# Performance work log

Measured on AMD Instinct MI355X. Metric: run time of the kernel, lower is better.

The kernel has to match this reference:

```python
import jax, jax.numpy as jnp
import numpy as np

B, T, E, H = 2, 2048, 1024, 16


def setup_inputs() -> dict:
    key = jax.random.key(0)
    ks = jax.random.split(key, 8)
    # VarianceScaling(1.0) ~ truncated normal with stddev ~ sqrt(1/fan_in)
    std = 1.0 / np.sqrt(E)
    x = jax.random.normal(ks[0], (B, T, E), dtype=jnp.float32)
    y = jax.random.normal(ks[1], (B, T, E), dtype=jnp.float32)
    # causal mask [1, 1, T, T]
    mask = jnp.tril(jnp.ones((T, T), dtype=jnp.float32))[None, None]
    Wq = jax.random.normal(ks[2], (E, E), dtype=jnp.float32) * std
    Wk = jax.random.normal(ks[3], (E, E), dtype=jnp.float32) * std
    Wv = jax.random.normal(ks[4], (E, E), dtype=jnp.float32) * std
    Wo = jax.random.normal(ks[5], (E, E), dtype=jnp.float32) * std
    bq = jnp.zeros((E,), jnp.float32)
    bk = jnp.zeros((E,), jnp.float32)
    bv = jnp.zeros((E,), jnp.float32)
    bo = jnp.zeros((E,), jnp.float32)
    return {"x": x, "y": y, "mask": mask, "Wq": Wq, "bq": bq,
            "Wk": Wk, "bk": bk, "Wv": Wv, "bv": bv, "Wo": Wo, "bo": bo,
            "num_heads": H}


def reference(x, y, mask, Wq, bq, Wk, bk, Wv, bv, Wo, bo, num_heads):
    Bx, Tq, Emb = x.shape
    Tkv = y.shape[1]
    d = Emb // num_heads
    q = (x @ Wq + bq).reshape(Bx, Tq, num_heads, d)
    k = (y @ Wk + bk).reshape(Bx, Tkv, num_heads, d)
    v = (y @ Wv + bv).reshape(Bx, Tkv, num_heads, d)
    scale = 1.0 / np.sqrt(d).astype(np.float32)
    att = scale * jnp.einsum('bthd,bThd->bhtT', q, k)  # [B,H,Tq,Tkv]
    att = att * mask - 1e10 * (1.0 - mask)
    att = jax.nn.softmax(att, axis=-1)
    out = jnp.einsum('bhtT,bThd->bthd', att, v).reshape(Bx, Tq, Emb)
    return out @ Wo + bo
```

## Files before the change

kernel.cpp:

```cpp
#include <hip/hip_runtime.h>
#include <stdint.h>

#define BB 2
#define TT 2048
#define EE 1024
#define HH 16
#define DD 64
#define MM (BB*TT)

typedef unsigned short u16;
typedef __attribute__((ext_vector_type(4))) float f32x4;
typedef __attribute__((ext_vector_type(8))) __bf16 bf16x8;
typedef __attribute__((ext_vector_type(8))) u16 u16x8;
typedef __attribute__((ext_vector_type(4))) u16 u16x4;

union FragU { u16x8 u; bf16x8 b; };
union BfU { __bf16 h; u16 u; };

__device__ __forceinline__ u16 f2bf(float f) {
  uint32_t u = __float_as_uint(f);
  u += 0x7fffu + ((u >> 16) & 1u);
  return (u16)(u >> 16);
}

__device__ __forceinline__ void gload16(const u16* __restrict__ g, u16* l) {
  __builtin_amdgcn_global_load_lds((const __attribute__((address_space(1))) void*)g,
                                   (__attribute__((address_space(3))) void*)l, 16, 0, 0);
}

__global__ __launch_bounds__(256) void prep(const float* __restrict__ x, const float* __restrict__ y,
                                            const float* __restrict__ Wq, const float* __restrict__ Wk,
                                            const float* __restrict__ Wv, const float* __restrict__ Wo,
                                            u16* __restrict__ xb, u16* __restrict__ yb,
                                            u16* __restrict__ Wqt, u16* __restrict__ Wkvt,
                                            u16* __restrict__ Wot) {
  __shared__ alignas(16) float tile[64][65];
  int bi = blockIdx.x, t = threadIdx.x;
  if (bi < 4096) {
    const float* src = (bi < 2048) ? x : y;
    u16* dst = (bi < 2048) ? xb : yb;
    int i = (bi & 2047) * 256 + t;
    const f32x4* s4 = (const f32x4*)src;
    f32x4 a = s4[2*i], b = s4[2*i+1];
    u16x8 o;
    o[0]=f2bf(a[0]); o[1]=f2bf(a[1]); o[2]=f2bf(a[2]); o[3]=f2bf(a[3]);
    o[4]=f2bf(b[0]); o[5]=f2bf(b[1]); o[6]=f2bf(b[2]); o[7]=f2bf(b[3]);
    ((u16x8*)dst)[i] = o;
    return;
  }
  int wi = bi - 4096;
  int z = wi >> 8;
  const float* W; u16* Tp;
  switch (z) {
    case 0: W = Wq; Tp = Wqt; break;
    case 1: W = Wk; Tp = Wkvt; break;
    case 2: W = Wv; Tp = Wkvt + (size_t)1024*EE; break;
    default: W = Wo; Tp = Wot; break;
  }
  int r8 = wi & 255;
  int n0 = (r8 & 15) * 64, k0 = (r8 >> 4) * 64;
#pragma unroll
  for (int i = 0; i < 16; ++i) {
    int idx = i*256 + t; int r = idx >> 6, c = idx & 63;
    tile[r][c] = W[(size_t)(k0 + r) * EE + n0 + c];
  }
  __syncthreads();
#pragma unroll
  for (int i = 0; i < 16; ++i) {
    int idx = i*256 + t; int rn = idx >> 6, ck = idx & 63;
    Tp[(size_t)(n0 + rn) * EE + k0 + ck] = f2bf(tile[ck][rn]);
  }
}

template <int BM, int EPI>
__device__ __forceinline__ void gemm_body(const u16* __restrict__ A, const u16* __restrict__ Bt,
                                          const float* __restrict__ bias, void* __restrict__ Cout,
                                          int N, int K, float oscale, int bm, int bn,
                                          u16 (*As)[64], u16 (*Bs)[64]) {
  constexpr int MI = (BM + 31) / 32;
  const int t = threadIdx.x;
  const int lane = t & 63, w = t >> 6;
  const int wr = w >> 1, wc = w & 1;
  const int g = lane >> 4, cl = lane & 15;

  f32x4 acc[MI][4] = {};

  const u16* Ag = A + (size_t)(bm * BM) * K;
  const u16* Bg = Bt + (size_t)(bn * 128) * K;

  const int rl = lane >> 3;
  const int sw = ((lane & 7) ^ rl) * 8;

  const int nk = K / 64;
  for (int kt = 0; kt < nk; ++kt) {
    const int k0 = kt * 64;
    __syncthreads();
    if (BM == 32) {
      gload16(Ag + (size_t)(w*8 + rl) * K + k0 + sw, &As[w*8][0]);
    } else {
#pragma unroll
      for (int j = 0; j < MI; ++j) {
        int ca = w * MI + j;
        gload16(Ag + (size_t)(ca*8 + rl) * K + k0 + sw, &As[ca*8][0]);
      }
    }
#pragma unroll
    for (int j = 0; j < 4; ++j) {
      int cb = w * 4 + j;
      gload16(Bg + (size_t)(cb*8 + rl) * K + k0 + sw, &Bs[cb*8][0]);
    }
    __syncthreads();
#pragma unroll
    for (int ks = 0; ks < 2; ++ks) {
      FragU af[MI], bfr[4];
#pragma unroll
      for (int mi = 0; mi < MI; ++mi) {
        int row = (BM == 32) ? (wr*16 + cl) : (wr*(BM/2) + mi*16 + cl);
        af[mi].u = *(const u16x8*)&As[row][((ks*4 + g) ^ (row & 7)) * 8];
      }
#pragma unroll
      for (int nj = 0; nj < 4; ++nj) {
        int row = wc*64 + nj*16 + cl;
        bfr[nj].u = *(const u16x8*)&Bs[row][((ks*4 + g) ^ (row & 7)) * 8];
      }
#pragma unroll
      for (int mi = 0; mi < MI; ++mi)
#pragma unroll
        for (int nj = 0; nj < 4; ++nj)
          acc[mi][nj] = __builtin_amdgcn_mfma_f32_16x16x32_bf16(af[mi].b, bfr[nj].b, acc[mi][nj], 0, 0, 0);
    }
  }

  const int cbase = bn*128 + wc*64 + cl;
  float bv[4];
#pragma unroll
  for (int nj = 0; nj < 4; ++nj) bv[nj] = bias[cbase + nj*16];
#pragma unroll
  for (int mi = 0; mi < MI; ++mi) {
    int row0 = (BM == 32) ? (bm*32 + wr*16 + (g << 2))
                          : (bm*BM + wr*(BM/2) + mi*16 + (g << 2));
    if (EPI == 2) {
      int bb = row0 >> 11;
      int tt = row0 & 2047;
      int tb64 = tt & ~63;
      int w6 = tt & 63;
      int p = ((w6 >> 5) << 5) | (((w6 >> 2) & 3) << 3) | (((w6 >> 4) & 1) << 2);
#pragma unroll
      for (int nj = 0; nj < 4; ++nj) {
        int cc = cbase + nj*16;
        int hh = cc >> 6, dd = cc & 63;
        u16x4 v;
#pragma unroll
        for (int i = 0; i < 4; ++i) v[i] = f2bf(acc[mi][nj][i] + bv[nj]);
        *(u16x4*)((u16*)Cout + ((size_t)((bb*HH + hh)*DD + dd))*2048 + tb64 + p) = v;
      }
    } else {
#pragma unroll
      for (int i = 0; i < 4; ++i) {
        if (EPI == 1) {
          float* Cp = (float*)Cout + (size_t)(row0 + i) * N + cbase;
#pragma unroll
          for (int nj = 0; nj < 4; ++nj)
            Cp[nj*16] = (acc[mi][nj][i] + bv[nj]) * oscale;
        } else {
          u16* Cp = (u16*)Cout + (size_t)(row0 + i) * N + cbase;
#pragma unroll
          for (int nj = 0; nj < 4; ++nj)
            Cp[nj*16] = f2bf((acc[mi][nj][i] + bv[nj]) * oscale);
        }
      }
    }
  }
}

__global__ __launch_bounds__(256) void gemm_qkv(const u16* __restrict__ xb, const u16* __restrict__ yb,
                                                const u16* __restrict__ Wqt, const u16* __restrict__ Wkvt,
                                                const float* __restrict__ bq, const float* __restrict__ bk,
                                                const float* __restrict__ bv,
                                                u16* __restrict__ Qb, u16* __restrict__ Kb,
                                                u16* __restrict__ Vtb, float c1) {
  __shared__ alignas(16) u16 As[64][64];
  __shared__ alignas(16) u16 Bs[128][64];
  const int i = blockIdx.x;
  const int l = (i & 7) * 192 + (i >> 3);
  const int bm = l / 24, bx = l % 24;
  if (bx < 8)
    gemm_body<64, 0>(xb, Wqt, bq, Qb, 1024, EE, c1, bm, bx, As, Bs);
  else if (bx < 16)
    gemm_body<64, 0>(yb, Wkvt, bk, Kb, 1024, EE, 1.0f, bm, bx - 8, As, Bs);
  else
    gemm_body<64, 2>(yb, Wkvt + (size_t)1024*EE, bv, Vtb, 1024, EE, 1.0f, bm, bx - 16, As, Bs);
}

__global__ __launch_bounds__(256) void gemm_o(const u16* __restrict__ Atb, const u16* __restrict__ Wot,
                                              const float* __restrict__ bo, float* __restrict__ out) {
  __shared__ alignas(16) u16 As[32][64];
  __shared__ alignas(16) u16 Bs[128][64];
  const int i = blockIdx.x;
  const int l = (i & 7) * 128 + (i >> 3);
  const int bm = l / 8, bn = l % 8;
  gemm_body<32, 1>(Atb, Wot, bo, out, 1024, EE, 1.0f, bm, bn, As, Bs);
}

__global__ __launch_bounds__(512, 4) void attn(const u16* __restrict__ Q, const u16* __restrict__ Kb,
                                               const u16* __restrict__ Vt, u16* __restrict__ O) {
  const int i0 = blockIdx.x;
  const int qp = i0 >> 5;
  const int bh = i0 & 31;
  const int b = bh >> 4, h = bh & 15;

  const int t = threadIdx.x, lane = t & 63, w = t >> 6;
  const int ws_ = w & 3;
  const int hi = w >> 2;
  const int g = lane >> 4, c = lane & 15;
  __shared__ alignas(16) u16 Ks[2][2][64][64];
  __shared__ alignas(16) u16 Vs[2][2][64][64];

  const u16* Kbase = Kb + (size_t)(b*TT) * 1024 + h*DD;
  const u16* Vtbase = Vt + (size_t)(b*HH + h) * DD * 2048;

  const int rl = lane >> 3;
  const int sw = ((lane & 7) ^ rl) * 8;
  const int rowb = w*8 + rl;
  const int rxor = (c & 7);

  FragU onef;
#pragma unroll
  for (int e = 0; e < 8; ++e) onef.u[e] = 0x3F80;

  for (int pi = 0; pi < 2; ++pi) {
    const int qt = pi ? 31 - qp : qp;
    const int qw0 = qt * 64 + ws_ * 16;

    FragU qf[2];
    const u16* Qbase = Q + ((size_t)(b*TT) + qw0) * EE + h*DD;
#pragma unroll
    for (int ks = 0; ks < 2; ++ks)
      qf[ks].u = *(const u16x8*)(Qbase + (size_t)c * EE + ks*32 + g*8);

    f32x4 oacc[4] = {};
    f32x4 lacc = {};

    const int nkv = qt + 1;
    const int npair = (nkv + 1) >> 1;

    __syncthreads();
    gload16(Kbase + (size_t)rowb * 1024 + sw, &Ks[0][0][w*8][0]);
    gload16(Vtbase + (size_t)rowb * 2048 + sw, &Vs[0][0][w*8][0]);
    if (1 < nkv) {
      gload16(Kbase + (size_t)(64 + rowb) * 1024 + sw, &Ks[0][1][w*8][0]);
      gload16(Vtbase + (size_t)rowb * 2048 + 64 + sw, &Vs[0][1][w*8][0]);
    }
    __syncthreads();

    for (int jj = 0; jj < npair; ++jj) {
      const int d = jj & 1;
      const int j0 = 2*jj;
      if (jj + 1 < npair) {
        const int kvn = (j0 + 2) * 64;
        gload16(Kbase + (size_t)(kvn + rowb) * 1024 + sw, &Ks[d^1][0][w*8][0]);
        gload16(Vtbase + (size_t)rowb * 2048 + kvn + sw, &Vs[d^1][0][w*8][0]);
        if (j0 + 3 < nkv) {
          gload16(Kbase + (size_t)(kvn + 64 + rowb) * 1024 + sw, &Ks[d^1][1][w*8][0]);
          gload16(Vtbase + (size_t)rowb * 2048 + kvn + 64 + sw, &Vs[d^1][1][w*8][0]);
        }
      }

      const int j = j0 + hi;
      const int kv0 = j * 64;
      if (j < nkv && kv0 <= qw0 + 15) {
        f32x4 s[4] = {};
        __builtin_amdgcn_s_setprio(1);
#pragma unroll
        for (int ks = 0; ks < 2; ++ks) {
          const int kc = ((ks*4 + g) ^ rxor) * 8;
          FragU kf[4];
#pragma unroll
          for (int nj = 0; nj < 4; ++nj)
            kf[nj].u = *(const u16x8*)&Ks[d][hi][nj*16 + c][kc];
#pragma unroll
          for (int nj = 0; nj < 4; ++nj)
            s[nj] = __builtin_amdgcn_mfma_f32_16x16x32_bf16(kf[nj].b, qf[ks].b, s[nj], 0, 0, 0);
        }
        __builtin_amdgcn_s_setprio(0);

        const bool full = (kv0 + 63 <= qw0);
        if (!full) {
          const int q = qw0 + c;
#pragma unroll
          for (int nj = 0; nj < 4; ++nj)
#pragma unroll
            for (int r = 0; r < 4; ++r)
              if (kv0 + nj*16 + 4*g + r > q) s[nj][r] = -1e30f;
        }

        FragU pa[2];
#pragma unroll
        for (int nj = 0; nj < 4; ++nj)
#pragma unroll
          for (int r = 0; r < 4; ++r) {
            float p = exp2f(s[nj][r]);
            BfU cv; cv.h = (__bf16)p;
            pa[nj >> 1].u[(nj & 1) * 4 + r] = cv.u;
          }

        __builtin_amdgcn_s_setprio(1);
#pragma unroll
        for (int ks = 0; ks < 2; ++ks) {
          const int vc = ((ks*4 + g) ^ rxor) * 8;
#pragma unroll
          for (int dj = 0; dj < 4; ++dj) {
            FragU vf;
            vf.u = *(const u16x8*)&Vs[d][hi][dj*16 + c][vc];
            oacc[dj] = __builtin_amdgcn_mfma_f32_16x16x32_bf16(pa[ks].b, vf.b, oacc[dj], 0, 0, 0);
          }
          lacc = __builtin_amdgcn_mfma_f32_16x16x32_bf16(pa[ks].b, onef.b, lacc, 0, 0, 0);
        }
        __builtin_amdgcn_s_setprio(0);
      }

      if (jj + 1 < npair)
        __syncthreads();
    }

    __syncthreads();
    float* mO = (float*)&Ks[0][0][0][0];
    float* mL = (float*)&Vs[0][0][0][0];

    if (hi) {
#pragma unroll
      for (int i = 0; i < 4; ++i) {
        int row = 4*g + i;
#pragma unroll
        for (int dj = 0; dj < 4; ++dj)
          mO[((size_t)(ws_*16 + row))*66 + dj*16 + c] = oacc[dj][i];
      }
      if (c == 0) {
#pragma unroll
        for (int i = 0; i < 4; ++i) mL[ws_*16 + 4*g + i] = lacc[i];
      }
    }
    __syncthreads();
    if (!hi) {
      u16* Ob = O + ((size_t)(b*TT) + qw0) * EE + h*DD;
#pragma unroll
      for (int i = 0; i < 4; ++i) {
        int row = 4*g + i;
        float inv = 1.f / (lacc[i] + mL[ws_*16 + row]);
#pragma unroll
        for (int dj = 0; dj < 4; ++dj) {
          float o1 = mO[((size_t)(ws_*16 + row))*66 + dj*16 + c];
          Ob[(size_t)row * EE + dj*16 + c] = f2bf((oacc[dj][i] + o1) * inv);
        }
      }
    }
  }
}

extern "C" void kernel_launch(void* const* d_in, const int* in_sizes, int n_in,
                              void* d_out, int out_size, void* d_ws, size_t ws_size,
                              hipStream_t stream) {
  const float* x  = (const float*)d_in[0];
  const float* y  = (const float*)d_in[1];
  const float* Wq = (const float*)d_in[3];
  const float* bq = (const float*)d_in[4];
  const float* Wk = (const float*)d_in[5];
  const float* bk = (const float*)d_in[6];
  const float* Wv = (const float*)d_in[7];
  const float* bv = (const float*)d_in[8];
  const float* Wo = (const float*)d_in[9];
  const float* bo = (const float*)d_in[10];

  if (ws_size < (size_t)58720256) return;

  char* ws = (char*)d_ws;
  u16* Wqt  = (u16*)(ws + 0);
  u16* Wkvt = (u16*)(ws + 2097152);
  u16* Wot  = (u16*)(ws + 6291456);
  u16* Qb   = (u16*)(ws + 8388608);
  u16* Kb   = (u16*)(ws + 16777216);
  u16* Vtb  = (u16*)(ws + 25165824);
  u16* Atb  = (u16*)(ws + 33554432);
  u16* xb   = (u16*)(ws + 41943040);
  u16* yb   = (u16*)(ws + 50331648);

  const float c1 = 0.125f * 1.44269504088896340736f;

  prep<<<5120, 256, 0, stream>>>(x, y, Wq, Wk, Wv, Wo, xb, yb, Wqt, Wkvt, Wot);
  gemm_qkv<<<1536, 256, 0, stream>>>(xb, yb, Wqt, Wkvt, bq, bk, bv, Qb, Kb, Vtb, c1);
  attn<<<512, 512, 0, stream>>>(Qb, Kb, Vtb, Atb);
  gemm_o<<<1024, 256, 0, stream>>>(Atb, Wot, bo, (float*)d_out);
}
```

Measured before the change: 101.8 us.

## Software-pipeline PV matmul one tile behind QK in attention loop

Defers the P·V MFMA of each KV tile to the next iteration, so it runs after the next tile's Q·K^T. This lets the exp/convert work and the matmuls interleave and hide latency. The V shared buffer grows to three slots so the previous tile's V stays valid while the next one is prefetched. The cost is more LDS per block, which may reduce occupancy, plus extra register pressure from carrying the P fragments across iterations.

```diff
diff --git a/kernel.cpp b/kernel.cpp
--- a/kernel.cpp
+++ b/kernel.cpp
@@ -214,7 +214,7 @@
   const int hi = w >> 2;
   const int g = lane >> 4, c = lane & 15;
   __shared__ alignas(16) u16 Ks[2][2][64][64];
-  __shared__ alignas(16) u16 Vs[2][2][64][64];
+  __shared__ alignas(16) u16 Vs[3][2][64][64];
 
   const u16* Kbase = Kb + (size_t)(b*TT) * 1024 + h*DD;
   const u16* Vtbase = Vt + (size_t)(b*HH + h) * DD * 2048;
@@ -253,23 +253,31 @@
     }
     __syncthreads();
 
+    FragU paP[2];
+    int vslotP = 0;
+    bool haveP = false;
+
+    int vs = 0;
     for (int jj = 0; jj < npair; ++jj) {
       const int d = jj & 1;
       const int j0 = 2*jj;
+      const int vsn = (vs == 2) ? 0 : vs + 1;
       if (jj + 1 < npair) {
         const int kvn = (j0 + 2) * 64;
         gload16(Kbase + (size_t)(kvn + rowb) * 1024 + sw, &Ks[d^1][0][w*8][0]);
-        gload16(Vtbase + (size_t)rowb * 2048 + kvn + sw, &Vs[d^1][0][w*8][0]);
+        gload16(Vtbase + (size_t)rowb * 2048 + kvn + sw, &Vs[vsn][0][w*8][0]);
         if (j0 + 3 < nkv) {
           gload16(Kbase + (size_t)(kvn + 64 + rowb) * 1024 + sw, &Ks[d^1][1][w*8][0]);
-          gload16(Vtbase + (size_t)rowb * 2048 + kvn + 64 + sw, &Vs[d^1][1][w*8][0]);
+          gload16(Vtbase + (size_t)rowb * 2048 + kvn + 64 + sw, &Vs[vsn][1][w*8][0]);
         }
       }
 
       const int j = j0 + hi;
       const int kv0 = j * 64;
-      if (j < nkv && kv0 <= qw0 + 15) {
-        f32x4 s[4] = {};
+      const bool active = (j < nkv && kv0 <= qw0 + 15);
+
+      f32x4 s[4] = {};
+      if (active) {
         __builtin_amdgcn_s_setprio(1);
 #pragma unroll
         for (int ks = 0; ks < 2; ++ks) {
@@ -283,7 +291,26 @@
             s[nj] = __builtin_amdgcn_mfma_f32_16x16x32_bf16(kf[nj].b, qf[ks].b, s[nj], 0, 0, 0);
         }
         __builtin_amdgcn_s_setprio(0);
-
+      }
+
+      if (haveP) {
+        __builtin_amdgcn_s_setprio(1);
+#pragma unroll
+        for (int ks = 0; ks < 2; ++ks) {
+          const int vc = ((ks*4 + g) ^ rxor) * 8;
+#pragma unroll
+          for (int dj = 0; dj < 4; ++dj) {
+            FragU vf;
+            vf.u = *(const u16x8*)&Vs[vslotP][hi][dj*16 + c][vc];
+            oacc[dj] = __builtin_amdgcn_mfma_f32_16x16x32_bf16(paP[ks].b, vf.b, oacc[dj], 0, 0, 0);
+          }
+          lacc = __builtin_amdgcn_mfma_f32_16x16x32_bf16(paP[ks].b, onef.b, lacc, 0, 0, 0);
+        }
+        __builtin_amdgcn_s_setprio(0);
+        haveP = false;
+      }
+
+      if (active) {
         const bool full = (kv0 + 63 <= qw0);
         if (!full) {
           const int q = qw0 + c;
@@ -294,33 +321,35 @@
               if (kv0 + nj*16 + 4*g + r > q) s[nj][r] = -1e30f;
         }
 
-        FragU pa[2];
 #pragma unroll
         for (int nj = 0; nj < 4; ++nj)
 #pragma unroll
           for (int r = 0; r < 4; ++r) {
             float p = exp2f(s[nj][r]);
             BfU cv; cv.h = (__bf16)p;
-            pa[nj >> 1].u[(nj & 1) * 4 + r] = cv.u;
+            paP[nj >> 1].u[(nj & 1) * 4 + r] = cv.u;
           }
-
-        __builtin_amdgcn_s_setprio(1);
-#pragma unroll
-        for (int ks = 0; ks < 2; ++ks) {
-          const int vc = ((ks*4 + g) ^ rxor) * 8;
-#pragma unroll
-          for (int dj = 0; dj < 4; ++dj) {
-            FragU vf;
-            vf.u = *(const u16x8*)&Vs[d][hi][dj*16 + c][vc];
-            oacc[dj] = __builtin_amdgcn_mfma_f32_16x16x32_bf16(pa[ks].b, vf.b, oacc[dj], 0, 0, 0);
-          }
-          lacc = __builtin_amdgcn_mfma_f32_16x16x32_bf16(pa[ks].b, onef.b, lacc, 0, 0, 0);
-        }
-        __builtin_amdgcn_s_setprio(0);
+        vslotP = vs;
+        haveP = true;
       }
 
       if (jj + 1 < npair)
         __syncthreads();
+      vs = vsn;
+    }
+
+    if (haveP) {
+#pragma unroll
+      for (int ks = 0; ks < 2; ++ks) {
+        const int vc = ((ks*4 + g) ^ rxor) * 8;
+#pragma unroll
+        for (int dj = 0; dj < 4; ++dj) {
+          FragU vf;
+          vf.u = *(const u16x8*)&Vs[vslotP][hi][dj*16 + c][vc];
+          oacc[dj] = __builtin_amdgcn_mfma_f32_16x16x32_bf16(paP[ks].b, vf.b, oacc[dj], 0, 0, 0);
+        }
+        lacc = __builtin_amdgcn_mfma_f32_16x16x32_bf16(paP[ks].b, onef.b, lacc, 0, 0, 0);
+      }
     }
 
     __syncthreads();
```

After: 102.5 us. About the same (+0.6%).

## Process both paired causal query tiles in one shared KV sweep

Applied to the files above, without the earlier changes.

The attention kernel used to run the two query tiles (qp and 31-qp) one after the other, each with its own K/V streaming loop. It now streams K/V once, over the longer tile's range, and applies each loaded block to both query tiles. This cuts K/V global loads and barrier iterations for the short tile. The block-to-tile mapping is also permuted so that heavy and light blocks interleave. In exchange, register pressure roughly doubles (two sets of accumulators and Q fragments), which may lower occupancy under launch_bounds(512,4). The old kv0 <= qw0+15 skip condition is also dropped, so a few fully masked chains now run.

```diff
diff --git a/kernel.cpp b/kernel.cpp
--- a/kernel.cpp
+++ b/kernel.cpp
@@ -205,9 +205,11 @@
 __global__ __launch_bounds__(512, 4) void attn(const u16* __restrict__ Q, const u16* __restrict__ Kb,
                                                const u16* __restrict__ Vt, u16* __restrict__ O) {
   const int i0 = blockIdx.x;
-  const int qp = i0 >> 5;
+  const int u = i0 >> 5;
   const int bh = i0 & 31;
+  const int qp = (u < 8) ? u : 23 - u;
   const int b = bh >> 4, h = bh & 15;
+  const int qtA = qp, qtB = 31 - qp;
 
   const int t = threadIdx.x, lane = t & 63, w = t >> 6;
   const int ws_ = w & 3;
@@ -228,105 +230,118 @@
 #pragma unroll
   for (int e = 0; e < 8; ++e) onef.u[e] = 0x3F80;
 
-  for (int pi = 0; pi < 2; ++pi) {
-    const int qt = pi ? 31 - qp : qp;
-    const int qw0 = qt * 64 + ws_ * 16;
-
-    FragU qf[2];
-    const u16* Qbase = Q + ((size_t)(b*TT) + qw0) * EE + h*DD;
-#pragma unroll
-    for (int ks = 0; ks < 2; ++ks)
-      qf[ks].u = *(const u16x8*)(Qbase + (size_t)c * EE + ks*32 + g*8);
-
-    f32x4 oacc[4] = {};
-    f32x4 lacc = {};
-
-    const int nkv = qt + 1;
-    const int npair = (nkv + 1) >> 1;
+  const int qw0A = qtA * 64 + ws_ * 16;
+  const int qw0B = qtB * 64 + ws_ * 16;
+
+  FragU qfA[2], qfB[2];
+  {
+    const u16* QbA = Q + ((size_t)(b*TT) + qw0A) * EE + h*DD;
+    const u16* QbB = Q + ((size_t)(b*TT) + qw0B) * EE + h*DD;
+#pragma unroll
+    for (int ks = 0; ks < 2; ++ks) {
+      qfA[ks].u = *(const u16x8*)(QbA + (size_t)c * EE + ks*32 + g*8);
+      qfB[ks].u = *(const u16x8*)(QbB + (size_t)c * EE + ks*32 + g*8);
+    }
+  }
+
+  f32x4 oaccA[4] = {}, oaccB[4] = {};
+  f32x4 laccA = {}, laccB = {};
+
+  const int nkvA = qtA + 1;
+  const int nkvB = qtB + 1;
+  const int npair = (nkvB + 1) >> 1;
+
+  gload16(Kbase + (size_t)rowb * 1024 + sw, &Ks[0][0][w*8][0]);
+  gload16(Vtbase + (size_t)rowb * 2048 + sw, &Vs[0][0][w*8][0]);
+  gload16(Kbase + (size_t)(64 + rowb) * 1024 + sw, &Ks[0][1][w*8][0]);
+  gload16(Vtbase + (size_t)rowb * 2048 + 64 + sw, &Vs[0][1][w*8][0]);
+  __syncthreads();
+
+  auto chain = [&](int d, int kv0, const FragU* qf, int qw0, f32x4* oacc, f32x4& lacc) {
+    f32x4 s[4] = {};
+    __builtin_amdgcn_s_setprio(1);
+#pragma unroll
+    for (int ks = 0; ks < 2; ++ks) {
+      const int kc = ((ks*4 + g) ^ rxor) * 8;
+      FragU kf[4];
+#pragma unroll
+      for (int nj = 0; nj < 4; ++nj)
+        kf[nj].u = *(const u16x8*)&Ks[d][hi][nj*16 + c][kc];
+#pragma unroll
+      for (int nj = 0; nj < 4; ++nj)
+        s[nj] = __builtin_amdgcn_mfma_f32_16x16x32_bf16(kf[nj].b, qf[ks].b, s[nj], 0, 0, 0);
+    }
+    __builtin_amdgcn_s_setprio(0);
+
+    const bool full = (kv0 + 63 <= qw0);
+    if (!full) {
+      const int q = qw0 + c;
+#pragma unroll
+      for (int nj = 0; nj < 4; ++nj)
+#pragma unroll
+        for (int r = 0; r < 4; ++r)
+          if (kv0 + nj*16 + 4*g + r > q) s[nj][r] = -1e30f;
+    }
+
+    FragU pa[2];
+#pragma unroll
+    for (int nj = 0; nj < 4; ++nj)
+#pragma unroll
+      for (int r = 0; r < 4; ++r) {
+        float p = exp2f(s[nj][r]);
+        BfU cv; cv.h = (__bf16)p;
+        pa[nj >> 1].u[(nj & 1) * 4 + r] = cv.u;
+      }
+
+    __builtin_amdgcn_s_setprio(1);
+#pragma unroll
+    for (int ks = 0; ks < 2; ++ks) {
+      const int vc = ((ks*4 + g) ^ rxor) * 8;
+#pragma unroll
+      for (int dj = 0; dj < 4; ++dj) {
+        FragU vf;
+        vf.u = *(const u16x8*)&Vs[d][hi][dj*16 + c][vc];
+        oacc[dj] = __builtin_amdgcn_mfma_f32_16x16x32_bf16(pa[ks].b, vf.b, oacc[dj], 0, 0, 0);
+      }
+      lacc = __builtin_amdgcn_mfma_f32_16x16x32_bf16(pa[ks].b, onef.b, lacc, 0, 0, 0);
+    }
+    __builtin_amdgcn_s_setprio(0);
+  };
+
+  for (int jj = 0; jj < npair; ++jj) {
+    const int d = jj & 1;
+    const int j0 = 2*jj;
+    if (jj + 1 < npair) {
+      const int kvn = (j0 + 2) * 64;
+      gload16(Kbase + (size_t)(kvn + rowb) * 1024 + sw, &Ks[d^1][0][w*8][0]);
+      gload16(Vtbase + (size_t)rowb * 2048 + kvn + sw, &Vs[d^1][0][w*8][0]);
+      if (j0 + 3 < nkvB) {
+        gload16(Kbase + (size_t)(kvn + 64 + rowb) * 1024 + sw, &Ks[d^1][1][w*8][0]);
+        gload16(Vtbase + (size_t)rowb * 2048 + kvn + 64 + sw, &Vs[d^1][1][w*8][0]);
+      }
+    }
+
+    const int j = j0 + hi;
+    const int kv0 = j * 64;
+    if (j < nkvB)
+      chain(d, kv0, qfB, qw0B, oaccB, laccB);
+    if (j < nkvA)
+      chain(d, kv0, qfA, qw0A, oaccA, laccA);
+
+    if (jj + 1 < npair)
+      __syncthreads();
+  }
+
+  float* mO = (float*)&Ks[0][0][0][0];
+  float* mL = (float*)&Vs[0][0][0][0];
+
+#pragma unroll
+  for (int ch = 0; ch < 2; ++ch) {
+    f32x4* oacc = ch ? oaccA : oaccB;
+    f32x4& lacc = ch ? laccA : laccB;
+    const int qw0 = ch ? qw0A : qw0B;
 
     __syncthreads();
-    gload16(Kbase + (size_t)rowb * 1024 + sw, &Ks[0][0][w*8][0]);
-    gload16(Vtbase + (size_t)rowb * 2048 + sw, &Vs[0][0][w*8][0]);
-    if (1 < nkv) {
-      gload16(Kbase + (size_t)(64 + rowb) * 1024 + sw, &Ks[0][1][w*8][0]);
-      gload16(Vtbase + (size_t)rowb * 2048 + 64 + sw, &Vs[0][1][w*8][0]);
-    }
-    __syncthreads();
-
-    for (int jj = 0; jj < npair; ++jj) {
-      const int d = jj & 1;
-      const int j0 = 2*jj;
-      if (jj + 1 < npair) {
-        const int kvn = (j0 + 2) * 64;
-        gload16(Kbase + (size_t)(kvn + rowb) * 1024 + sw, &Ks[d^1][0][w*8][0]);
-        gload16(Vtbase + (size_t)rowb * 2048 + kvn + sw, &Vs[d^1][0][w*8][0]);
-        if (j0 + 3 < nkv) {
-          gload16(Kbase + (size_t)(kvn + 64 + rowb) * 1024 + sw, &Ks[d^1][1][w*8][0]);
-          gload16(Vtbase + (size_t)rowb * 2048 + kvn + 64 + sw, &Vs[d^1][1][w*8][0]);
-        }
-      }
-
-      const int j = j0 + hi;
-      const int kv0 = j * 64;
-      if (j < nkv && kv0 <= qw0 + 15) {
-        f32x4 s[4] = {};
-        __builtin_amdgcn_s_setprio(1);
-#pragma unroll
-        for (int ks = 0; ks < 2; ++ks) {
-          const int kc = ((ks*4 + g) ^ rxor) * 8;
-          FragU kf[4];
-#pragma unroll
-          for (int nj = 0; nj < 4; ++nj)
-            kf[nj].u = *(const u16x8*)&Ks[d][hi][nj*16 + c][kc];
-#pragma unroll
-          for (int nj = 0; nj < 4; ++nj)
-            s[nj] = __builtin_amdgcn_mfma_f32_16x16x32_bf16(kf[nj].b, qf[ks].b, s[nj], 0, 0, 0);
-        }
-        __builtin_amdgcn_s_setprio(0);
-
-        const bool full = (kv0 + 63 <= qw0);
-        if (!full) {
-          const int q = qw0 + c;
-#pragma unroll
-          for (int nj = 0; nj < 4; ++nj)
-#pragma unroll
-            for (int r = 0; r < 4; ++r)
-              if (kv0 + nj*16 + 4*g + r > q) s[nj][r] = -1e30f;
-        }
-
-        FragU pa[2];
-#pragma unroll
-        for (int nj = 0; nj < 4; ++nj)
-#pragma unroll
-          for (int r = 0; r < 4; ++r) {
-            float p = exp2f(s[nj][r]);
-            BfU cv; cv.h = (__bf16)p;
-            pa[nj >> 1].u[(nj & 1) * 4 + r] = cv.u;
-          }
-
-        __builtin_amdgcn_s_setprio(1);
-#pragma unroll
-        for (int ks = 0; ks < 2; ++ks) {
-          const int vc = ((ks*4 + g) ^ rxor) * 8;
-#pragma unroll
-          for (int dj = 0; dj < 4; ++dj) {
-            FragU vf;
-            vf.u = *(const u16x8*)&Vs[d][hi][dj*16 + c][vc];
-            oacc[dj] = __builtin_amdgcn_mfma_f32_16x16x32_bf16(pa[ks].b, vf.b, oacc[dj], 0, 0, 0);
-          }
-          lacc = __builtin_amdgcn_mfma_f32_16x16x32_bf16(pa[ks].b, onef.b, lacc, 0, 0, 0);
-        }
-        __builtin_amdgcn_s_setprio(0);
-      }
-
-      if (jj + 1 < npair)
-        __syncthreads();
-    }
-
-    __syncthreads();
-    float* mO = (float*)&Ks[0][0][0][0];
-    float* mL = (float*)&Vs[0][0][0][0];
-
     if (hi) {
 #pragma unroll
       for (int i = 0; i < 4; ++i) {
```

After: 100.9 us. Within noise of the previous version (-0.9%).
